# Optimization experiments

Measured on AMD Instinct MI355X. Metric: run time of the kernel, lower is better.

Reference implementation:

```python
import jax, jax.numpy as jnp
import numpy as np

B, S, H, IN, OUT = 1024, 512, 512, 2, 2


def setup_inputs() -> dict:
    key = jax.random.key(0)
    ks = jax.random.split(key, 10)
    s = 1.0 / np.sqrt(H)  # torch default uniform init scale for GRU/Linear
    u = lambda k, shp: jax.random.uniform(k, shp, jnp.float32, -s, s)
    return {
        "X0": jax.random.normal(ks[0], (B, OUT), jnp.float32),
        "V": jax.random.normal(ks[1], (B, S, IN), jnp.float32),
        "W_ih": u(ks[2], (3 * H, IN + OUT)),
        "W_hh": u(ks[3], (3 * H, H)),
        "b_ih": u(ks[4], (3 * H,)),
        "b_hh": u(ks[5], (3 * H,)),
        "W1": u(ks[6], (H // 2, H)),
        "b1": u(ks[7], (H // 2,)),
        "W2": u(ks[8], (OUT, H // 2)),
        "b2": u(ks[9], (OUT,)),
    }


def reference(X0, V, W_ih, W_hh, b_ih, b_hh, W1, b1, W2, b2):
    out_size = W2.shape[0]
    hidden = W_hh.shape[1]

    def step(carry, v_t):
        x_prev, h_prev = carry  # [B,out], [B,H]
        linear_pred = x_prev + v_t[:, :out_size]
        gru_in = jnp.concatenate([v_t, x_prev], axis=-1)  # [B, in+out]
        gi = gru_in @ W_ih.T + b_ih  # [B, 3H]
        gh = h_prev @ W_hh.T + b_hh  # [B, 3H]
        i_r, i_z, i_n = jnp.split(gi, 3, axis=-1)
        h_r, h_z, h_n = jnp.split(gh, 3, axis=-1)
        r = jax.nn.sigmoid(i_r + h_r)
        z = jax.nn.sigmoid(i_z + h_z)
        n = jnp.tanh(i_n + r * h_n)
        h_t = (1.0 - z) * n + z * h_prev  # torch GRU cell update
        residual = jax.nn.relu(h_t @ W1.T + b1) @ W2.T + b2
        x_t = linear_pred + residual
        return (x_t, h_t), x_t

    h0 = jnp.zeros((X0.shape[0], hidden), X0.dtype)
    _, xs = jax.lax.scan(step, (X0, h0), jnp.swapaxes(V, 0, 1))  # xs: [S,B,out]
    return jnp.swapaxes(xs, 0, 1)  # [B,S,out]
```

## Files before the change

### kernel.cpp

```cpp
#include <hip/hip_runtime.h>

#define Ssz 512
#define BT  64
#define SLC 32

typedef __attribute__((ext_vector_type(8))) short short8;
typedef __attribute__((ext_vector_type(4))) float f32x4;
typedef __attribute__((ext_vector_type(2))) float f32x2;
typedef __attribute__((ext_vector_type(4))) unsigned uint4v;
typedef __attribute__((ext_vector_type(2))) unsigned uint2v;

#define WS_PW   0u
#define WS_PW1  1572864u
#define WS_HB   1835008u
#define WS_PX   3932160u
#define WS_BAR  4456448u

__device__ __forceinline__ unsigned short f2bf(float f) {
  unsigned int u = __builtin_bit_cast(unsigned int, f);
  u += 0x7fffu + ((u >> 16) & 1u);
  return (unsigned short)(u >> 16);
}
__device__ __forceinline__ float sigm(float x) {
  x = fminf(fmaxf(x, -30.f), 30.f);
  return 1.f / (1.f + __expf(-x));
}
__device__ __forceinline__ float tanh_f(float x) {
  x = fminf(fmaxf(x, -15.f), 15.f);
  float e = __expf(2.f * x);
  return (e - 1.f) / (e + 1.f);
}

__device__ __forceinline__ uint4v gload16(const void* p) {
  uint4v d;
  asm volatile("global_load_dwordx4 %0, %1, off sc0 sc1" : "=v"(d) : "v"(p));
  return d;
}
__device__ __forceinline__ unsigned gload4(const void* p) {
  unsigned d;
  asm volatile("global_load_dword %0, %1, off sc0 sc1" : "=v"(d) : "v"(p));
  return d;
}
__device__ __forceinline__ void gstore16(void* p, uint4v v) {
  asm volatile("global_store_dwordx4 %0, %1, off sc0 sc1" :: "v"(p), "v"(v) : "memory");
}
__device__ __forceinline__ void gstore4(void* p, unsigned v) {
  asm volatile("global_store_dword %0, %1, off sc0 sc1" :: "v"(p), "v"(v) : "memory");
}
__device__ __forceinline__ void vwait0() {
  asm volatile("s_waitcnt vmcnt(0)" ::: "memory");
  __builtin_amdgcn_sched_barrier(0);
}

__global__ void pack_whh_k(const float* __restrict__ Wp, unsigned short* __restrict__ dst,
                           unsigned* __restrict__ barz) {
  if (blockIdx.x == 0) {
    for (int i = threadIdx.x; i < 1024; i += 256) barz[i] = 0u;
  }
  int T = blockIdx.x * 256 + threadIdx.x;
  int l  = T & 63;
  int r1 = T >> 6;
  int kk = r1 & 15;
  int r2 = r1 >> 4;
  int q  = r2 % 6;
  int sl = r2 / 6;
  int g = q >> 1, ch = q & 1;
  int j  = g * 512 + sl * 32 + ch * 16 + (l & 15);
  int kb = kk * 32 + (l >> 4) * 8;
  const float* src = Wp + j * 512 + kb;
  short8 o;
#pragma unroll
  for (int e = 0; e < 8; ++e) o[e] = (short)f2bf(src[e]);
  *reinterpret_cast<short8*>(dst + (size_t)T * 8) = o;
}

__global__ void pack_w1_k(const float* __restrict__ W1, unsigned short* __restrict__ dst) {
  int T = blockIdx.x * 256 + threadIdx.x;
  int l  = T & 63;
  int r1 = T >> 6;
  int kk = r1 & 15;
  int sl = r1 >> 4;
  int j  = sl * 16 + (l & 15);
  int kb = kk * 32 + (l >> 4) * 8;
  const float* src = W1 + j * 512 + kb;
  short8 o;
#pragma unroll
  for (int e = 0; e < 8; ++e) o[e] = (short)f2bf(src[e]);
  *reinterpret_cast<short8*>(dst + (size_t)T * 8) = o;
}

__device__ __forceinline__ int haddr(int rowbase, int sw, int ld, int kk) {
  return rowbase + (((ld << 4) + (kk << 6)) ^ sw);
}

__global__ __launch_bounds__(256, 1) void gru_main(
    const float* __restrict__ X0, const float* __restrict__ V,
    const float* __restrict__ Wih, const float* __restrict__ bih,
    const float* __restrict__ bhh, const float* __restrict__ b1,
    const float* __restrict__ W2, const float* __restrict__ b2,
    const unsigned short* __restrict__ PW, const unsigned short* __restrict__ PW1,
    unsigned short* __restrict__ Hb, float* __restrict__ px,
    unsigned* __restrict__ bar, float* __restrict__ out)
{
  __shared__ alignas(16) unsigned short hfull[BT * 512];
  __shared__ alignas(16) unsigned short hstage[BT][40];
  __shared__ alignas(16) float xg[BT][4];

  const int tid = threadIdx.x;
  const int l  = tid & 63, w = tid >> 6;
  const int lm = l & 15,  ld = l >> 4;
  const int rt = blockIdx.x & 15, sl = blockIdx.x >> 4;
  const int rfh = w >> 1, ch = w & 1;
  const int row0 = rt * BT;
  char* hfullB = reinterpret_cast<char*>(hfull);

  unsigned* fl1 = bar + rt * 32;
  unsigned* fl2 = fl1 + 16;

  short8 BW[3][16];
  {
    const char* pwb = reinterpret_cast<const char*>(PW);
#pragma unroll
    for (int g = 0; g < 3; ++g)
#pragma unroll
      for (int kk = 0; kk < 16; ++kk)
        BW[g][kk] = *reinterpret_cast<const short8*>(
            pwb + (size_t)((((sl * 6 + g * 2 + ch) * 16 + kk) * 64 + l) * 16));
  }
  short8 BM[16];
  {
    const char* pw1b = reinterpret_cast<const char*>(PW1);
#pragma unroll
    for (int kk = 0; kk < 16; ++kk)
      BM[kk] = *reinterpret_cast<const short8*>(
          pw1b + (size_t)(((sl * 16 + kk) * 64 + l) * 16));
  }

  const int jcol = sl * SLC + ch * 16 + lm;
  f32x4 wvx[3]; float bi[3], bh[3];
#pragma unroll
  for (int g = 0; g < 3; ++g) {
    int jg = g * 512 + jcol;
    wvx[g] = *reinterpret_cast<const f32x4*>(Wih + (size_t)jg * 4);
    bi[g] = bih[jg];
    bh[g] = bhh[jg];
  }
  const int ic = sl * 16 + lm;
  const float b1v = b1[ic];
  const float w2a = W2[ic], w2b = W2[256 + ic];
  const float b2c = b2[tid & 1];

  float xcur = 0.f;
  if (tid < BT * 2) {
    int row = tid >> 1, c = tid & 1;
    float x0 = X0[(row0 + row) * 2 + c];
    xcur = x0;
    xg[row][2 + c] = x0;
    xg[row][c] = V[(size_t)(row0 + row) * (Ssz * 2) + c];
  }
  float hp[2][4];
#pragma unroll
  for (int q = 0; q < 2; ++q)
#pragma unroll
    for (int r = 0; r < 4; ++r) hp[q][r] = 0.f;
  __syncthreads();

  const int rbA0 = (rfh * 32 + lm) * 1024,      swA0 = ((rfh * 32 + lm) & 7) << 4;
  const int rbA1 = (rfh * 32 + 16 + lm) * 1024, swA1 = ((rfh * 32 + 16 + lm) & 7) << 4;
  const int rbB  = (w * 16 + lm) * 1024,        swB  = ((w * 16 + lm) & 7) << 4;

  for (int i = 0; i <= Ssz; ++i) {
    f32x4 acc[2][3];
#pragma unroll
    for (int q = 0; q < 2; ++q)
#pragma unroll
      for (int g = 0; g < 3; ++g) acc[q][g] = (f32x4){0.f, 0.f, 0.f, 0.f};

    if (i > 0) {
      {
        const unsigned* fp = fl1 + (l & 15);
        for (;;) {
          unsigned v = gload4(fp);
          vwait0();
          if (__all((int)(v >= (unsigned)i))) break;
          __builtin_amdgcn_s_sleep(1);
        }
      }

      {
        const char* hsrc = reinterpret_cast<const char*>(
            Hb + (size_t)((i - 1) & 1) * (1024 * 512) + (size_t)row0 * 512);
        uint4v fb[16];
#pragma unroll
        for (int j = 0; j < 16; ++j)
          fb[j] = gload16(hsrc + (size_t)(w * 16 + j) * 1024 + l * 16);
        vwait0();
#pragma unroll
        for (int j = 0; j < 16; ++j) {
          const int m = w * 16 + j;
          *reinterpret_cast<uint4v*>(hfullB + m * 1024 + ((l * 16) ^ ((m & 7) << 4))) = fb[j];
        }
      }

      {
        f32x4 am = (f32x4){0.f, 0.f, 0.f, 0.f};
#pragma unroll
        for (int kk = 0; kk < 16; ++kk) {
          short8 a = *reinterpret_cast<const short8*>(hfullB + haddr(rbB, swB, ld, kk));
          am = __builtin_amdgcn_mfma_f32_16x16x32_bf16(a, BM[kk], am, 0, 0, 0);
        }
        float pa[4], pb[4];
#pragma unroll
        for (int r = 0; r < 4; ++r) {
          float mv = fmaxf(am[r] + b1v, 0.f);
          pa[r] = mv * w2a;
          pb[r] = mv * w2b;
        }
#pragma unroll
        for (int off = 1; off < 16; off <<= 1)
#pragma unroll
          for (int r = 0; r < 4; ++r) {
            pa[r] += __shfl_xor(pa[r], off);
            pb[r] += __shfl_xor(pb[r], off);
          }
        if (lm == 0) {
#pragma unroll
          for (int r = 0; r < 4; ++r) {
            int row = w * 16 + ld * 4 + r;
            float* p0 = px + ((size_t)(rt * 64 + row) * 2 + 0) * 16 + sl;
            float* p1 = px + ((size_t)(rt * 64 + row) * 2 + 1) * 16 + sl;
            gstore4(p0, __builtin_bit_cast(unsigned, pa[r]));
            gstore4(p1, __builtin_bit_cast(unsigned, pb[r]));
          }
        }
      }
      asm volatile("s_waitcnt vmcnt(0)" ::: "memory");
      __syncthreads();
      if (tid == 0) gstore4(fl2 + sl, (unsigned)i);

      if (i < Ssz) {
#pragma unroll
        for (int kk = 0; kk < 16; ++kk) {
          short8 a0 = *reinterpret_cast<const short8*>(hfullB + haddr(rbA0, swA0, ld, kk));
          short8 a1 = *reinterpret_cast<const short8*>(hfullB + haddr(rbA1, swA1, ld, kk));
          acc[0][0] = __builtin_amdgcn_mfma_f32_16x16x32_bf16(a0, BW[0][kk], acc[0][0], 0, 0, 0);
          acc[1][0] = __builtin_amdgcn_mfma_f32_16x16x32_bf16(a1, BW[0][kk], acc[1][0], 0, 0, 0);
          acc[0][1] = __builtin_amdgcn_mfma_f32_16x16x32_bf16(a0, BW[1][kk], acc[0][1], 0, 0, 0);
          acc[1][1] = __builtin_amdgcn_mfma_f32_16x16x32_bf16(a1, BW[1][kk], acc[1][1], 0, 0, 0);
          acc[0][2] = __builtin_amdgcn_mfma_f32_16x16x32_bf16(a0, BW[2][kk], acc[0][2], 0, 0, 0);
          acc[1][2] = __builtin_amdgcn_mfma_f32_16x16x32_bf16(a1, BW[2][kk], acc[1][2], 0, 0, 0);
        }
      }

      if (w < 2) {
        const unsigned* fp = fl2 + (l & 15);
        for (;;) {
          unsigned v = gload4(fp);
          vwait0();
          if (__all((int)(v >= (unsigned)i))) break;
          __builtin_amdgcn_s_sleep(1);
        }
      }
      if (tid < BT * 2) {
        int row = tid >> 1, c = tid & 1;
        const float* pc = px + ((size_t)(rt * 64 + row) * 2 + c) * 16;
        f32x4 s0 = __builtin_bit_cast(f32x4, gload16(pc + 0));
        f32x4 s1 = __builtin_bit_cast(f32x4, gload16(pc + 4));
        f32x4 s2 = __builtin_bit_cast(f32x4, gload16(pc + 8));
        f32x4 s3 = __builtin_bit_cast(f32x4, gload16(pc + 12));
        vwait0();
        float s = b2c;
#pragma unroll
        for (int r = 0; r < 4; ++r) s += s0[r] + s1[r] + s2[r] + s3[r];
        float vprev = xg[row][c];
        float xt = xcur + vprev + s;
        xcur = xt;
        if (sl == 0) out[(size_t)(row0 + row) * (Ssz * 2) + (i - 1) * 2 + c] = xt;
        xg[row][2 + c] = xt;
        xg[row][c] = (i < Ssz) ? V[(size_t)(row0 + row) * (Ssz * 2) + i * 2 + c] : 0.f;
      }
      __syncthreads();
    }

    if (i < Ssz) {
#pragma unroll
      for (int rf2 = 0; rf2 < 2; ++rf2) {
#pragma unroll
        for (int r = 0; r < 4; ++r) {
          const int m = rfh * 32 + rf2 * 16 + ld * 4 + r;
          const f32x4 xv = *reinterpret_cast<const f32x4*>(&xg[m][0]);
          float gv0 = wvx[0][0]*xv[0] + wvx[0][1]*xv[1] + wvx[0][2]*xv[2] + wvx[0][3]*xv[3];
          float gv1 = wvx[1][0]*xv[0] + wvx[1][1]*xv[1] + wvx[1][2]*xv[2] + wvx[1][3]*xv[3];
          float gv2 = wvx[2][0]*xv[0] + wvx[2][1]*xv[1] + wvx[2][2]*xv[2] + wvx[2][3]*xv[3];
          float rr = sigm(gv0 + bi[0] + bh[0] + acc[rf2][0][r]);
          float zz = sigm(gv1 + bi[1] + bh[1] + acc[rf2][1][r]);
          float nn = tanh_f(gv2 + bi[2] + rr * (acc[rf2][2][r] + bh[2]));
          float ht = (1.f - zz) * nn + zz * hp[rf2][r];
          hp[rf2][r] = ht;
          hstage[m][ch * 16 + lm] = f2bf(ht);
        }
      }
      __syncthreads();

      {
        int row = tid >> 2, seg = tid & 3;
        uint4v hv = *reinterpret_cast<const uint4v*>(&hstage[row][seg * 8]);
        gstore16(Hb + (size_t)(i & 1) * (1024 * 512)
                    + (size_t)(row0 + row) * 512 + sl * SLC + seg * 8, hv);
      }
      asm volatile("s_waitcnt vmcnt(0)" ::: "memory");
      __syncthreads();
      if (tid == 0) gstore4(fl1 + sl, (unsigned)(i + 1));
    }
  }
}

extern "C" void kernel_launch(void* const* d_in, const int* in_sizes, int n_in,
                              void* d_out, int out_size, void* d_ws, size_t ws_size,
                              hipStream_t stream) {
  const float* X0  = (const float*)d_in[0];
  const float* V   = (const float*)d_in[1];
  const float* Wih = (const float*)d_in[2];
  const float* Whh = (const float*)d_in[3];
  const float* bih = (const float*)d_in[4];
  const float* bhh = (const float*)d_in[5];
  const float* W1  = (const float*)d_in[6];
  const float* b1  = (const float*)d_in[7];
  const float* W2  = (const float*)d_in[8];
  const float* b2  = (const float*)d_in[9];
  float* out = (float*)d_out;

  char* ws = (char*)d_ws;
  unsigned short* PW  = (unsigned short*)(ws + WS_PW);
  unsigned short* PW1 = (unsigned short*)(ws + WS_PW1);
  unsigned short* Hb  = (unsigned short*)(ws + WS_HB);
  float*          px  = (float*)(ws + WS_PX);
  unsigned*       bar = (unsigned*)(ws + WS_BAR);

  pack_whh_k<<<384, 256, 0, stream>>>(Whh, PW, bar);
  pack_w1_k<<<64, 256, 0, stream>>>(W1, PW1);
  gru_main<<<256, 256, 0, stream>>>(X0, V, Wih, bih, bhh, b1, W2, b2,
                                    PW, PW1, Hb, px, bar, out);
}
```

Before: 3.931 ms.

## Replace block-wide barriers with per-wave flags and register-held x state

Each wave now publishes its own progress flag (four per slice) instead of one flag per block, and consumers poll all 64 per-wave flags. Per-wave hidden-state staging and the x/v values, which are kept in registers and broadcast with shuffles, replace the shared xg array. This removes three __syncthreads per step. The cost is more flag traffic and redundant px loads and reductions in every wave, and the lane-only ordering inside each wave's staging must stay correct.

```diff
diff --git a/kernel.cpp b/kernel.cpp
--- a/kernel.cpp
+++ b/kernel.cpp
@@ -6,9 +6,7 @@
 
 typedef __attribute__((ext_vector_type(8))) short short8;
 typedef __attribute__((ext_vector_type(4))) float f32x4;
-typedef __attribute__((ext_vector_type(2))) float f32x2;
 typedef __attribute__((ext_vector_type(4))) unsigned uint4v;
-typedef __attribute__((ext_vector_type(2))) unsigned uint2v;
 
 #define WS_PW   0u
 #define WS_PW1  1572864u
@@ -52,10 +50,19 @@
   __builtin_amdgcn_sched_barrier(0);
 }
 
+__device__ __forceinline__ void pollflags(const unsigned* fp, unsigned target) {
+  for (;;) {
+    unsigned v = gload4(fp);
+    vwait0();
+    if (__all((int)(v >= target))) break;
+    __builtin_amdgcn_s_sleep(1);
+  }
+}
+
 __global__ void pack_whh_k(const float* __restrict__ Wp, unsigned short* __restrict__ dst,
                            unsigned* __restrict__ barz) {
   if (blockIdx.x == 0) {
-    for (int i = threadIdx.x; i < 1024; i += 256) barz[i] = 0u;
+    for (int i = threadIdx.x; i < 2048; i += 256) barz[i] = 0u;
   }
   int T = blockIdx.x * 256 + threadIdx.x;
   int l  = T & 63;
@@ -103,8 +110,7 @@
     unsigned* __restrict__ bar, float* __restrict__ out)
 {
   __shared__ alignas(16) unsigned short hfull[BT * 512];
-  __shared__ alignas(16) unsigned short hstage[BT][40];
-  __shared__ alignas(16) float xg[BT][4];
+  __shared__ alignas(16) unsigned short hstage[4][32][16];
 
   const int tid = threadIdx.x;
   const int l  = tid & 63, w = tid >> 6;
@@ -114,8 +120,13 @@
   const int row0 = rt * BT;
   char* hfullB = reinterpret_cast<char*>(hfull);
 
-  unsigned* fl1 = bar + rt * 32;
-  unsigned* fl2 = fl1 + 16;
+  unsigned* fl1 = bar + rt * 64;
+  unsigned* fl2 = bar + 1024 + rt * 64;
+
+  const int pj = l & 31;
+  const int pidx = (pj >> 1) * 4 + (w & ~1) + (pj & 1);
+  const unsigned* p1 = fl1 + pidx;
+  const unsigned* p2 = fl2 + pidx;
 
   short8 BW[3][16];
   {
@@ -148,22 +159,18 @@
   const int ic = sl * 16 + lm;
   const float b1v = b1[ic];
   const float w2a = W2[ic], w2b = W2[256 + ic];
-  const float b2c = b2[tid & 1];
-
-  float xcur = 0.f;
-  if (tid < BT * 2) {
-    int row = tid >> 1, c = tid & 1;
-    float x0 = X0[(row0 + row) * 2 + c];
-    xcur = x0;
-    xg[row][2 + c] = x0;
-    xg[row][c] = V[(size_t)(row0 + row) * (Ssz * 2) + c];
-  }
+  const float b2c = b2[l & 1];
+
+  const int xrow = rfh * 32 + (l >> 1);
+  const int xc   = l & 1;
+  float xcur = X0[(row0 + xrow) * 2 + xc];
+  float vcur = V[(size_t)(row0 + xrow) * (Ssz * 2) + xc];
+
   float hp[2][4];
 #pragma unroll
   for (int q = 0; q < 2; ++q)
 #pragma unroll
     for (int r = 0; r < 4; ++r) hp[q][r] = 0.f;
-  __syncthreads();
 
   const int rbA0 = (rfh * 32 + lm) * 1024,      swA0 = ((rfh * 32 + lm) & 7) << 4;
   const int rbA1 = (rfh * 32 + 16 + lm) * 1024, swA1 = ((rfh * 32 + 16 + lm) & 7) << 4;
@@ -177,15 +184,7 @@
       for (int g = 0; g < 3; ++g) acc[q][g] = (f32x4){0.f, 0.f, 0.f, 0.f};
 
     if (i > 0) {
-      {
-        const unsigned* fp = fl1 + (l & 15);
-        for (;;) {
-          unsigned v = gload4(fp);
-          vwait0();
-          if (__all((int)(v >= (unsigned)i))) break;
-          __builtin_amdgcn_s_sleep(1);
-        }
-      }
+      pollflags(p1, (unsigned)i);
 
       {
         const char* hsrc = reinterpret_cast<const char*>(
@@ -228,15 +227,15 @@
           for (int r = 0; r < 4; ++r) {
             int row = w * 16 + ld * 4 + r;
             float* p0 = px + ((size_t)(rt * 64 + row) * 2 + 0) * 16 + sl;
-            float* p1 = px + ((size_t)(rt * 64 + row) * 2 + 1) * 16 + sl;
+            float* p1s = px + ((size_t)(rt * 64 + row) * 2 + 1) * 16 + sl;
             gstore4(p0, __builtin_bit_cast(unsigned, pa[r]));
-            gstore4(p1, __builtin_bit_cast(unsigned, pb[r]));
+            gstore4(p1s, __builtin_bit_cast(unsigned, pb[r]));
           }
         }
-      }
-      asm volatile("s_waitcnt vmcnt(0)" ::: "memory");
+        asm volatile("s_waitcnt vmcnt(0)" ::: "memory");
+        if (l == 0) gstore4(fl2 + sl * 4 + w, (unsigned)i);
+      }
       __syncthreads();
-      if (tid == 0) gstore4(fl2 + sl, (unsigned)i);
 
       if (i < Ssz) {
 #pragma unroll
@@ -252,18 +251,10 @@
         }
       }
 
-      if (w < 2) {
-        const unsigned* fp = fl2 + (l & 15);
-        for (;;) {
-          unsigned v = gload4(fp);
-          vwait0();
-          if (__all((int)(v >= (unsigned)i))) break;
-          __builtin_amdgcn_s_sleep(1);
-        }
-      }
-      if (tid < BT * 2) {
-        int row = tid >> 1, c = tid & 1;
-        const float* pc = px + ((size_t)(rt * 64 + row) * 2 + c) * 16;
+      pollflags(p2, (unsigned)i);
+
+      {
+        const float* pc = px + ((size_t)(rt * 64 + xrow) * 2 + xc) * 16;
         f32x4 s0 = __builtin_bit_cast(f32x4, gload16(pc + 0));
         f32x4 s1 = __builtin_bit_cast(f32x4, gload16(pc + 4));
         f32x4 s2 = __builtin_bit_cast(f32x4, gload16(pc + 8));
@@ -272,14 +263,12 @@
         float s = b2c;
 #pragma unroll
         for (int r = 0; r < 4; ++r) s += s0[r] + s1[r] + s2[r] + s3[r];
-        float vprev = xg[row][c];
-        float xt = xcur + vprev + s;
+        float xt = xcur + vcur + s;
         xcur = xt;
-        if (sl == 0) out[(size_t)(row0 + row) * (Ssz * 2) + (i - 1) * 2 + c] = xt;
-        xg[row][2 + c] = xt;
-        xg[row][c] = (i < Ssz) ? V[(size_t)(row0 + row) * (Ssz * 2) + i * 2 + c] : 0.f;
-      }
-      __syncthreads();
+        if (sl == 0 && ch == 0)
+          out[(size_t)(row0 + xrow) * (Ssz * 2) + (i - 1) * 2 + xc] = xt;
+        vcur = (i < Ssz) ? V[(size_t)(row0 + xrow) * (Ssz * 2) + i * 2 + xc] : 0.f;
+      }
     }
 
     if (i < Ssz) {
@@ -287,30 +276,32 @@
       for (int rf2 = 0; rf2 < 2; ++rf2) {
 #pragma unroll
         for (int r = 0; r < 4; ++r) {
-          const int m = rfh * 32 + rf2 * 16 + ld * 4 + r;
-          const f32x4 xv = *reinterpret_cast<const f32x4*>(&xg[m][0]);
-          float gv0 = wvx[0][0]*xv[0] + wvx[0][1]*xv[1] + wvx[0][2]*xv[2] + wvx[0][3]*xv[3];
-          float gv1 = wvx[1][0]*xv[0] + wvx[1][1]*xv[1] + wvx[1][2]*xv[2] + wvx[1][3]*xv[3];
-          float gv2 = wvx[2][0]*xv[0] + wvx[2][1]*xv[1] + wvx[2][2]*xv[2] + wvx[2][3]*xv[3];
+          const int rl = rf2 * 16 + ld * 4 + r;
+          float v0 = __shfl(vcur, rl * 2);
+          float v1 = __shfl(vcur, rl * 2 + 1);
+          float x0 = __shfl(xcur, rl * 2);
+          float x1 = __shfl(xcur, rl * 2 + 1);
+          float gv0 = wvx[0][0]*v0 + wvx[0][1]*v1 + wvx[0][2]*x0 + wvx[0][3]*x1;
+          float gv1 = wvx[1][0]*v0 + wvx[1][1]*v1 + wvx[1][2]*x0 + wvx[1][3]*x1;
+          float gv2 = wvx[2][0]*v0 + wvx[2][1]*v1 + wvx[2][2]*x0 + wvx[2][3]*x1;
           float rr = sigm(gv0 + bi[0] + bh[0] + acc[rf2][0][r]);
           float zz = sigm(gv1 + bi[1] + bh[1] + acc[rf2][1][r]);
           float nn = tanh_f(gv2 + bi[2] + rr * (acc[rf2][2][r] + bh[2]));
           float ht = (1.f - zz) * nn + zz * hp[rf2][r];
           hp[rf2][r] = ht;
-          hstage[m][ch * 16 + lm] = f2bf(ht);
-        }
-      }
-      __syncthreads();
-
+          hstage[w][rl][lm] = f2bf(ht);
+        }
+      }
       {
-        int row = tid >> 2, seg = tid & 3;
-        uint4v hv = *reinterpret_cast<const uint4v*>(&hstage[row][seg * 8]);
+        asm volatile("s_waitcnt lgkmcnt(0)" ::: "memory");
+        __builtin_amdgcn_sched_barrier(0);
+        const int prow = l >> 1, seg = l & 1;
+        uint4v hv = *reinterpret_cast<const uint4v*>(&hstage[w][prow][seg * 8]);
         gstore16(Hb + (size_t)(i & 1) * (1024 * 512)
-                    + (size_t)(row0 + row) * 512 + sl * SLC + seg * 8, hv);
-      }
-      asm volatile("s_waitcnt vmcnt(0)" ::: "memory");
-      __syncthreads();
-      if (tid == 0) gstore4(fl1 + sl, (unsigned)(i + 1));
+                    + (size_t)(row0 + rfh * 32 + prow) * 512 + sl * 32 + ch * 16 + seg * 8, hv);
+        asm volatile("s_waitcnt vmcnt(0)" ::: "memory");
+        if (l == 0) gstore4(fl1 + sl * 4 + w, (unsigned)(i + 1));
+      }
     }
   }
 }
```

Result: slower. 6.157 ms (+56.6%).

## Repartition GRU blocks into 16-row tiles with 4 column slices and LDS W1

Applied to the files above, without the earlier changes.

Changes the block decomposition from 16 row tiles by 16 hidden slices (64 rows, 32 columns each) to 64 row tiles by 4 slices (16 rows, 128 columns each). Each wave now owns 32 hidden columns for 16 rows, holding twice the W_hh fragments in registers, while the W1 fragments move into LDS. The goal is to shrink the per-step h gather per block and the cross-block flag fan-in from 16 to 4 blocks, cutting per-step synchronisation latency. In exchange each block does more MFMA work per step and the register pressure rises, which could cause spills.

```diff
diff --git a/kernel.cpp b/kernel.cpp
--- a/kernel.cpp
+++ b/kernel.cpp
@@ -1,14 +1,10 @@
 #include <hip/hip_runtime.h>
 
 #define Ssz 512
-#define BT  64
-#define SLC 32
 
 typedef __attribute__((ext_vector_type(8))) short short8;
 typedef __attribute__((ext_vector_type(4))) float f32x4;
-typedef __attribute__((ext_vector_type(2))) float f32x2;
 typedef __attribute__((ext_vector_type(4))) unsigned uint4v;
-typedef __attribute__((ext_vector_type(2))) unsigned uint2v;
 
 #define WS_PW   0u
 #define WS_PW1  1572864u
@@ -51,11 +47,19 @@
   asm volatile("s_waitcnt vmcnt(0)" ::: "memory");
   __builtin_amdgcn_sched_barrier(0);
 }
+__device__ __forceinline__ void pollflags(const unsigned* fp, unsigned target) {
+  for (;;) {
+    unsigned v = gload4(fp);
+    vwait0();
+    if (__all((int)(v >= target))) break;
+    __builtin_amdgcn_s_sleep(1);
+  }
+}
 
 __global__ void pack_whh_k(const float* __restrict__ Wp, unsigned short* __restrict__ dst,
                            unsigned* __restrict__ barz) {
   if (blockIdx.x == 0) {
-    for (int i = threadIdx.x; i < 1024; i += 256) barz[i] = 0u;
+    for (int i = threadIdx.x; i < 2048; i += 256) barz[i] = 0u;
   }
   int T = blockIdx.x * 256 + threadIdx.x;
   int l  = T & 63;
@@ -63,9 +67,9 @@
   int kk = r1 & 15;
   int r2 = r1 >> 4;
   int q  = r2 % 6;
-  int sl = r2 / 6;
+  int slO = r2 / 6;
   int g = q >> 1, ch = q & 1;
-  int j  = g * 512 + sl * 32 + ch * 16 + (l & 15);
+  int j  = g * 512 + slO * 32 + ch * 16 + (l & 15);
   int kb = kk * 32 + (l >> 4) * 8;
   const float* src = Wp + j * 512 + kb;
   short8 o;
@@ -79,18 +83,14 @@
   int l  = T & 63;
   int r1 = T >> 6;
   int kk = r1 & 15;
-  int sl = r1 >> 4;
-  int j  = sl * 16 + (l & 15);
+  int hb = r1 >> 4;
+  int j  = hb * 16 + (l & 15);
   int kb = kk * 32 + (l >> 4) * 8;
   const float* src = W1 + j * 512 + kb;
   short8 o;
 #pragma unroll
   for (int e = 0; e < 8; ++e) o[e] = (short)f2bf(src[e]);
   *reinterpret_cast<short8*>(dst + (size_t)T * 8) = o;
-}
-
-__device__ __forceinline__ int haddr(int rowbase, int sw, int ld, int kk) {
-  return rowbase + (((ld << 4) + (kk << 6)) ^ sw);
 }
 
 __global__ __launch_bounds__(256, 1) void gru_main(
@@ -102,61 +102,63 @@
     unsigned short* __restrict__ Hb, float* __restrict__ px,
     unsigned* __restrict__ bar, float* __restrict__ out)
 {
-  __shared__ alignas(16) unsigned short hfull[BT * 512];
-  __shared__ alignas(16) unsigned short hstage[BT][40];
-  __shared__ alignas(16) float xg[BT][4];
+  __shared__ alignas(16) unsigned short hfull[16 * 512];
+  __shared__ alignas(16) char w1lds[65536];
+  __shared__ alignas(16) unsigned short hstage[16][136];
+  __shared__ alignas(16) float xg[16][4];
 
   const int tid = threadIdx.x;
   const int l  = tid & 63, w = tid >> 6;
   const int lm = l & 15,  ld = l >> 4;
-  const int rt = blockIdx.x & 15, sl = blockIdx.x >> 4;
-  const int rfh = w >> 1, ch = w & 1;
-  const int row0 = rt * BT;
+  const int rt = blockIdx.x & 63, sl = blockIdx.x >> 6;
+  const int row0 = rt * 16;
   char* hfullB = reinterpret_cast<char*>(hfull);
 
-  unsigned* fl1 = bar + rt * 32;
-  unsigned* fl2 = fl1 + 16;
-
-  short8 BW[3][16];
+  unsigned* fl1 = bar + rt * 4;
+  unsigned* fl2 = bar + 1024 + rt * 4;
+
+  short8 BW[2][3][16];
   {
-    const char* pwb = reinterpret_cast<const char*>(PW);
-#pragma unroll
-    for (int g = 0; g < 3; ++g)
-#pragma unroll
-      for (int kk = 0; kk < 16; ++kk)
-        BW[g][kk] = *reinterpret_cast<const short8*>(
-            pwb + (size_t)((((sl * 6 + g * 2 + ch) * 16 + kk) * 64 + l) * 16));
-  }
-  short8 BM[16];
+    const short8* pws = reinterpret_cast<const short8*>(PW);
+#pragma unroll
+    for (int ct = 0; ct < 2; ++ct)
+#pragma unroll
+      for (int g = 0; g < 3; ++g)
+#pragma unroll
+        for (int kk = 0; kk < 16; ++kk)
+          BW[ct][g][kk] = pws[(size_t)((((sl * 4 + w) * 6 + g * 2 + ct) * 16 + kk) * 64 + l)];
+  }
   {
-    const char* pw1b = reinterpret_cast<const char*>(PW1);
-#pragma unroll
-    for (int kk = 0; kk < 16; ++kk)
-      BM[kk] = *reinterpret_cast<const short8*>(
-          pw1b + (size_t)(((sl * 16 + kk) * 64 + l) * 16));
-  }
-
-  const int jcol = sl * SLC + ch * 16 + lm;
-  f32x4 wvx[3]; float bi[3], bh[3];
-#pragma unroll
-  for (int g = 0; g < 3; ++g) {
-    int jg = g * 512 + jcol;
-    wvx[g] = *reinterpret_cast<const f32x4*>(Wih + (size_t)jg * 4);
-    bi[g] = bih[jg];
-    bh[g] = bhh[jg];
-  }
-  const int ic = sl * 16 + lm;
+    const short8* pw1s = reinterpret_cast<const short8*>(PW1);
+#pragma unroll
+    for (int kk = 0; kk < 16; ++kk) {
+      short8 v = pw1s[(size_t)(((sl * 4 + w) * 16 + kk) * 64 + l)];
+      *reinterpret_cast<short8*>(w1lds + (size_t)((w * 16 + kk) * 1024 + l * 16)) = v;
+    }
+  }
+
+  f32x4 wvx[2][3]; float bi[2][3], bh[2][3];
+#pragma unroll
+  for (int ct = 0; ct < 2; ++ct)
+#pragma unroll
+    for (int g = 0; g < 3; ++g) {
+      int jg = g * 512 + sl * 128 + w * 32 + ct * 16 + lm;
+      wvx[ct][g] = *reinterpret_cast<const f32x4*>(Wih + (size_t)jg * 4);
+      bi[ct][g] = bih[jg];
+      bh[ct][g] = bhh[jg];
+    }
+  const int ic = (sl * 4 + w) * 16 + lm;
   const float b1v = b1[ic];
   const float w2a = W2[ic], w2b = W2[256 + ic];
-  const float b2c = b2[tid & 1];
-
-  float xcur = 0.f;
-  if (tid < BT * 2) {
+  const float b2c = b2[l & 1];
+
+  float xcur = 0.f, vcur = 0.f;
+  if (tid < 32) {
     int row = tid >> 1, c = tid & 1;
-    float x0 = X0[(row0 + row) * 2 + c];
-    xcur = x0;
-    xg[row][2 + c] = x0;
-    xg[row][c] = V[(size_t)(row0 + row) * (Ssz * 2) + c];
+    xcur = X0[(row0 + row) * 2 + c];
+    vcur = V[(size_t)(row0 + row) * 1024 + c];
+    xg[row][c] = vcur;
+    xg[row][2 + c] = xcur;
   }
   float hp[2][4];
 #pragma unroll
@@ -165,9 +167,7 @@
     for (int r = 0; r < 4; ++r) hp[q][r] = 0.f;
   __syncthreads();
 
-  const int rbA0 = (rfh * 32 + lm) * 1024,      swA0 = ((rfh * 32 + lm) & 7) << 4;
-  const int rbA1 = (rfh * 32 + 16 + lm) * 1024, swA1 = ((rfh * 32 + 16 + lm) & 7) << 4;
-  const int rbB  = (w * 16 + lm) * 1024,        swB  = ((w * 16 + lm) & 7) << 4;
+  const int rbA = lm * 1024, swA = (lm & 7) << 4;
 
   for (int i = 0; i <= Ssz; ++i) {
     f32x4 acc[2][3];
@@ -177,37 +177,32 @@
       for (int g = 0; g < 3; ++g) acc[q][g] = (f32x4){0.f, 0.f, 0.f, 0.f};
 
     if (i > 0) {
-      {
-        const unsigned* fp = fl1 + (l & 15);
-        for (;;) {
-          unsigned v = gload4(fp);
-          vwait0();
-          if (__all((int)(v >= (unsigned)i))) break;
-          __builtin_amdgcn_s_sleep(1);
-        }
-      }
+      pollflags(fl1 + (l & 3), (unsigned)i);
 
       {
         const char* hsrc = reinterpret_cast<const char*>(
             Hb + (size_t)((i - 1) & 1) * (1024 * 512) + (size_t)row0 * 512);
-        uint4v fb[16];
-#pragma unroll
-        for (int j = 0; j < 16; ++j)
-          fb[j] = gload16(hsrc + (size_t)(w * 16 + j) * 1024 + l * 16);
+        uint4v fb[4];
+#pragma unroll
+        for (int j = 0; j < 4; ++j)
+          fb[j] = gload16(hsrc + (size_t)(tid + 256 * j) * 16);
         vwait0();
 #pragma unroll
-        for (int j = 0; j < 16; ++j) {
-          const int m = w * 16 + j;
-          *reinterpret_cast<uint4v*>(hfullB + m * 1024 + ((l * 16) ^ ((m & 7) << 4))) = fb[j];
-        }
-      }
+        for (int j = 0; j < 4; ++j) {
+          const int c = tid + 256 * j;
+          const int row = c >> 6, c16 = c & 63;
+          *reinterpret_cast<uint4v*>(hfullB + row * 1024 + ((c16 * 16) ^ ((row & 7) << 4))) = fb[j];
+        }
+      }
+      __syncthreads();
 
       {
         f32x4 am = (f32x4){0.f, 0.f, 0.f, 0.f};
 #pragma unroll
         for (int kk = 0; kk < 16; ++kk) {
-          short8 a = *reinterpret_cast<const short8*>(hfullB + haddr(rbB, swB, ld, kk));
-          am = __builtin_amdgcn_mfma_f32_16x16x32_bf16(a, BM[kk], am, 0, 0, 0);
+          short8 a = *reinterpret_cast<const short8*>(hfullB + rbA + ((ld * 16 + kk * 64) ^ swA));
+          short8 b = *reinterpret_cast<const short8*>(w1lds + (w * 16 + kk) * 1024 + l * 16);
+          am = __builtin_amdgcn_mfma_f32_16x16x32_bf16(a, b, am, 0, 0, 0);
         }
         float pa[4], pb[4];
 #pragma unroll
@@ -224,13 +219,14 @@
             pb[r] += __shfl_xor(pb[r], off);
           }
         if (lm == 0) {
+          const int slot = sl * 4 + w;
 #pragma unroll
           for (int r = 0; r < 4; ++r) {
-            int row = w * 16 + ld * 4 + r;
-            float* p0 = px + ((size_t)(rt * 64 + row) * 2 + 0) * 16 + sl;
-            float* p1 = px + ((size_t)(rt * 64 + row) * 2 + 1) * 16 + sl;
-            gstore4(p0, __builtin_bit_cast(unsigned, pa[r]));
-            gstore4(p1, __builtin_bit_cast(unsigned, pb[r]));
+            int row = ld * 4 + r;
+            gstore4(px + ((size_t)(rt * 16 + row) * 2 + 0) * 16 + slot,
+                    __builtin_bit_cast(unsigned, pa[r]));
+            gstore4(px + ((size_t)(rt * 16 + row) * 2 + 1) * 16 + slot,
+                    __builtin_bit_cast(unsigned, pb[r]));
           }
         }
       }
@@ -241,29 +237,21 @@
       if (i < Ssz) {
 #pragma unroll
         for (int kk = 0; kk < 16; ++kk) {
-          short8 a0 = *reinterpret_cast<const short8*>(hfullB + haddr(rbA0, swA0, ld, kk));
-          short8 a1 = *reinterpret_cast<const short8*>(hfullB + haddr(rbA1, swA1, ld, kk));
-          acc[0][0] = __builtin_amdgcn_mfma_f32_16x16x32_bf16(a0, BW[0][kk], acc[0][0], 0, 0, 0);
-          acc[1][0] = __builtin_amdgcn_mfma_f32_16x16x32_bf16(a1, BW[0][kk], acc[1][0], 0, 0, 0);
-          acc[0][1] = __builtin_amdgcn_mfma_f32_16x16x32_bf16(a0, BW[1][kk], acc[0][1], 0, 0, 0);
-          acc[1][1] = __builtin_amdgcn_mfma_f32_16x16x32_bf16(a1, BW[1][kk], acc[1][1], 0, 0, 0);
-          acc[0][2] = __builtin_amdgcn_mfma_f32_16x16x32_bf16(a0, BW[2][kk], acc[0][2], 0, 0, 0);
-          acc[1][2] = __builtin_amdgcn_mfma_f32_16x16x32_bf16(a1, BW[2][kk], acc[1][2], 0, 0, 0);
-        }
-      }
-
-      if (w < 2) {
-        const unsigned* fp = fl2 + (l & 15);
-        for (;;) {
-          unsigned v = gload4(fp);
-          vwait0();
-          if (__all((int)(v >= (unsigned)i))) break;
-          __builtin_amdgcn_s_sleep(1);
-        }
-      }
-      if (tid < BT * 2) {
+          short8 a = *reinterpret_cast<const short8*>(hfullB + rbA + ((ld * 16 + kk * 64) ^ swA));
+          acc[0][0] = __builtin_amdgcn_mfma_f32_16x16x32_bf16(a, BW[0][0][kk], acc[0][0], 0, 0, 0);
+          acc[1][0] = __builtin_amdgcn_mfma_f32_16x16x32_bf16(a, BW[1][0][kk], acc[1][0], 0, 0, 0);
+          acc[0][1] = __builtin_amdgcn_mfma_f32_16x16x32_bf16(a, BW[0][1][kk], acc[0][1], 0, 0, 0);
+          acc[1][1] = __builtin_amdgcn_mfma_f32_16x16x32_bf16(a, BW[1][1][kk], acc[1][1], 0, 0, 0);
+          acc[0][2] = __builtin_amdgcn_mfma_f32_16x16x32_bf16(a, BW[0][2][kk], acc[0][2], 0, 0, 0);
+          acc[1][2] = __builtin_amdgcn_mfma_f32_16x16x32_bf16(a, BW[1][2][kk], acc[1][2], 0, 0, 0);
+        }
+      }
+
+      if (w == 0) pollflags(fl2 + (l & 3), (unsigned)i);
+
+      if (tid < 32) {
         int row = tid >> 1, c = tid & 1;
-        const float* pc = px + ((size_t)(rt * 64 + row) * 2 + c) * 16;
+        const float* pc = px + ((size_t)(rt * 16 + row) * 2 + c) * 16;
         f32x4 s0 = __builtin_bit_cast(f32x4, gload16(pc + 0));
         f32x4 s1 = __builtin_bit_cast(f32x4, gload16(pc + 4));
         f32x4 s2 = __builtin_bit_cast(f32x4, gload16(pc + 8));
@@ -272,41 +260,42 @@
         float s = b2c;
 #pragma unroll
         for (int r = 0; r < 4; ++r) s += s0[r] + s1[r] + s2[r] + s3[r];
-        float vprev = xg[row][c];
-        float xt = xcur + vprev + s;
+        float xt = xcur + vcur + s;
         xcur = xt;
-        if (sl == 0) out[(size_t)(row0 + row) * (Ssz * 2) + (i - 1) * 2 + c] = xt;
+        if ((row >> 2) == sl)
+          out[(size_t)(row0 + row) * 1024 + (i - 1) * 2 + c] = xt;
+        vcur = (i < Ssz) ? V[(size_t)(row0 + row) * 1024 + i * 2 + c] : 0.f;
+        xg[row][c] = vcur;
         xg[row][2 + c] = xt;
-        xg[row][c] = (i < Ssz) ? V[(size_t)(row0 + row) * (Ssz * 2) + i * 2 + c] : 0.f;
       }
       __syncthreads();
     }
 
     if (i < Ssz) {
 #pragma unroll
-      for (int rf2 = 0; rf2 < 2; ++rf2) {
+      for (int ct = 0; ct < 2; ++ct) {
 #pragma unroll
         for (int r = 0; r < 4; ++r) {
-          const int m = rfh * 32 + rf2 * 16 + ld * 4 + r;
+          const int m = ld * 4 + r;
           const f32x4 xv = *reinterpret_cast<const f32x4*>(&xg[m][0]);
-          float gv0 = wvx[0][0]*xv[0] + wvx[0][1]*xv[1] + wvx[0][2]*xv[2] + wvx[0][3]*xv[3];
-          float gv1 = wvx[1][0]*xv[0] + wvx[1][1]*xv[1] + wvx[1][2]*xv[2] + wvx[1][3]*xv[3];
-          float gv2 = wvx[2][0]*xv[0] + wvx[2][1]*xv[1] + wvx[2][2]*xv[2] + wvx[2][3]*xv[3];
-          float rr = sigm(gv0 + bi[0] + bh[0] + acc[rf2][0][r]);
-          float zz = sigm(gv1 + bi[1] + bh[1] + acc[rf2][1][r]);
-          float nn = tanh_f(gv2 + bi[2] + rr * (acc[rf2][2][r] + bh[2]));
-          float ht = (1.f - zz) * nn + zz * hp[rf2][r];
-          hp[rf2][r] = ht;
-          hstage[m][ch * 16 + lm] = f2bf(ht);
+          float gv0 = wvx[ct][0][0]*xv[0] + wvx[ct][0][1]*xv[1] + wvx[ct][0][2]*xv[2] + wvx[ct][0][3]*xv[3];
+          float gv1 = wvx[ct][1][0]*xv[0] + wvx[ct][1][1]*xv[1] + wvx[ct][1][2]*xv[2] + wvx[ct][1][3]*xv[3];
+          float gv2 = wvx[ct][2][0]*xv[0] + wvx[ct][2][1]*xv[1] + wvx[ct][2][2]*xv[2] + wvx[ct][2][3]*xv[3];
+          float rr = sigm(gv0 + bi[ct][0] + bh[ct][0] + acc[ct][0][r]);
+          float zz = sigm(gv1 + bi[ct][1] + bh[ct][1] + acc[ct][1][r]);
+          float nn = tanh_f(gv2 + bi[ct][2] + rr * (acc[ct][2][r] + bh[ct][2]));
+          float ht = (1.f - zz) * nn + zz * hp[ct][r];
+          hp[ct][r] = ht;
+          hstage[m][w * 32 + ct * 16 + lm] = f2bf(ht);
         }
       }
       __syncthreads();
 
       {
-        int row = tid >> 2, seg = tid & 3;
+        int row = tid >> 4, seg = tid & 15;
         uint4v hv = *reinterpret_cast<const uint4v*>(&hstage[row][seg * 8]);
         gstore16(Hb + (size_t)(i & 1) * (1024 * 512)
-                    + (size_t)(row0 + row) * 512 + sl * SLC + seg * 8, hv);
+                    + (size_t)(row0 + row) * 512 + sl * 128 + seg * 8, hv);
       }
       asm volatile("s_waitcnt vmcnt(0)" ::: "memory");
       __syncthreads();
```

After: 4.635 ms. 17.9% more time.
